# Kernel tuning notes

Measured on AMD Instinct MI355X. Metric: run time of the kernel, lower is better.

## Reference

```python
import jax, jax.numpy as jnp
import numpy as np

E = 500_000
N = 50_000
F_IN = 128
F_OUT = 128


def setup_inputs() -> dict:
    key = jax.random.key(0)
    ks = jax.random.split(key, 6)
    src_feat = jax.random.normal(ks[0], (E, F_IN), dtype=jnp.float32)
    dst_feat = jax.random.normal(ks[1], (E, F_IN), dtype=jnp.float32)
    # sorted dst ids -> contiguous per-dst segments (edges grouped by dst, time-ordered within group)
    dst_np = np.sort(np.random.default_rng(0).integers(0, N, size=E)).astype(np.int64)
    seg_start = np.searchsorted(dst_np, dst_np, side='left')  # first edge index of each edge's segment
    e_idx = np.arange(E)
    u = np.random.default_rng(1).random(E)
    # dst_max_eid: index of last edge (within same dst group) with time <= this edge's time
    dst_max_eid_np = (seg_start + np.floor(u * (e_idx - seg_start + 1))).astype(np.int64)
    dst_deg_np = (dst_max_eid_np - seg_start + 1).astype(np.float32)
    gain = float(np.sqrt(2.0))  # relu gain, xavier_uniform
    lim = gain * np.sqrt(6.0 / (F_IN + F_OUT))
    W_self = jax.random.uniform(ks[2], (F_IN, F_OUT), minval=-lim, maxval=lim, dtype=jnp.float32)
    W_neigh = jax.random.uniform(ks[3], (F_IN, F_OUT), minval=-lim, maxval=lim, dtype=jnp.float32)
    return {
        'src_feat': src_feat,
        'dst_feat': dst_feat,
        'dst_ids': jnp.asarray(dst_np),
        'dst_max_eid': jnp.asarray(dst_max_eid_np),
        'dst_deg': jnp.asarray(dst_deg_np),
        'W_self': W_self,
        'b_self': jnp.zeros((F_OUT,), jnp.float32),
        'W_neigh': W_neigh,
        'b_neigh': jnp.zeros((F_OUT,), jnp.float32),
    }


def _segmented_cumsum(x, seg_ids):
    # seg_ids sorted ascending; per-segment inclusive prefix sum over edge axis
    cs = jnp.cumsum(x, axis=0)                                   # [E, F]
    seg_start = jnp.searchsorted(seg_ids, seg_ids, side='left')  # [E]
    cs_pad = jnp.concatenate([jnp.zeros((1, x.shape[1]), x.dtype), cs], axis=0)
    return cs - cs_pad[seg_start]                                # subtract prefix before segment


def reference(src_feat, dst_feat, dst_ids, dst_max_eid, dst_deg, W_self, b_self, W_neigh, b_neigh):
    # group_apply_edges(group_by='dst'): cumsum of src_feat within each dst segment ('mean' aggr)
    h_feat = _segmented_cumsum(src_feat, dst_ids)          # [E, F_in]
    h_neigh = h_feat[dst_max_eid]                          # gather running aggregate per edge
    mean_cof = dst_deg + 1.0
    h_neigh = h_neigh / mean_cof[:, None]
    rst = (dst_feat @ W_self + b_self) + (h_neigh @ W_neigh + b_neigh)
    return rst
```

## Files before the change

### kernel.cpp

```cpp
#include <hip/hip_runtime.h>
#include <hip/hip_bf16.h>


#define FDIM 128
#define NNODES 50000

typedef __attribute__((ext_vector_type(4))) float f32x4;
typedef __attribute__((ext_vector_type(2))) float f32x2;
typedef __attribute__((ext_vector_type(8))) short bf16x8;

static __device__ __forceinline__ float bf2f(unsigned short u) {
  union { unsigned int i; float f; } v; v.i = ((unsigned int)u) << 16; return v.f;
}
static __device__ __forceinline__ unsigned short f2bf(float f) {
  union { float f; unsigned int i; } v; v.f = f;
  unsigned int x = v.i;
  return (unsigned short)((x + 0x7fffu + ((x >> 16) & 1u)) >> 16);
}

__global__ __launch_bounds__(256) void pack_w_kernel(
    const float* __restrict__ Wself,
    const float* __restrict__ Wneigh,
    unsigned short* __restrict__ Wp)
{
  int t = blockIdx.x * blockDim.x + threadIdx.x;
  if (t >= 8 * 8 * 64) return;
  int l  = t & 63;
  int n0 = (t >> 6) & 7;
  int ks = t >> 9;
  int n = n0 * 16 + (l & 15);
  int kbase = ks * 32 + ((l >> 4) * 8);
  unsigned short outv[8] __attribute__((aligned(16)));
#pragma unroll
  for (int j = 0; j < 8; ++j) {
    int k = kbase + j;
    float w = (k < FDIM) ? Wself[k * FDIM + n] : Wneigh[(k - FDIM) * FDIM + n];
    outv[j] = f2bf(w);
  }
  ((uint4*)Wp)[t] = *(const uint4*)outv;
}

__global__ __launch_bounds__(256) void seg_start_kernel(
    const int* __restrict__ dst_ids,
    int* __restrict__ node_start,
    int E, int nnodes)
{
  int e = blockIdx.x * blockDim.x + threadIdx.x;
  if (e >= E) return;
  int d = dst_ids[e];
  int dprev = (e == 0) ? -1 : dst_ids[e - 1];
  for (int n = dprev + 1; n <= d; ++n) node_start[n] = e;
  if (e == E - 1) {
    for (int n = d + 1; n <= nnodes; ++n) node_start[n] = E;
  }
}

__global__ __launch_bounds__(256) void seg_cumsum_kernel(
    const float* __restrict__ src,
    const int* __restrict__ node_start,
    unsigned short* __restrict__ cs,
    int nnodes)
{
  int wave = (blockIdx.x * blockDim.x + threadIdx.x) >> 6;
  int lane = threadIdx.x & 63;
  if (wave >= nnodes) return;

  int s = node_start[wave];
  int e = node_start[wave + 1];
  if (s >= e) return;

  const float* sp = src + (size_t)s * FDIM + lane * 2;
  unsigned int* op = (unsigned int*)(cs + (size_t)s * FDIM + lane * 2);

  f32x2 v0 = *(const f32x2*)sp;
  f32x2 v1 = (s + 1 < e) ? *(const f32x2*)(sp + FDIM) : v0;
  float a0 = 0.f, a1 = 0.f;
  for (int j = s; j < e; ++j) {
    f32x2 vn = v1;
    if (j + 2 < e) vn = *(const f32x2*)(sp + (size_t)(j + 2 - s) * FDIM);
    a0 += v0.x;
    a1 += v0.y;
    unsigned int w = ((unsigned int)f2bf(a1) << 16) | (unsigned int)f2bf(a0);
    *op = w;
    op += FDIM / 2;
    v0 = v1;
    v1 = vn;
  }
}

__global__ __launch_bounds__(256) void gemm_kernel(
    const float* __restrict__ dstf,
    const unsigned short* __restrict__ cs,
    const int* __restrict__ dst_max_eid,
    const float* __restrict__ dst_deg,
    const unsigned short* __restrict__ Wp,
    const float* __restrict__ b_self,
    const float* __restrict__ b_neigh,
    float* __restrict__ out,
    int E)
{
  int lane = threadIdx.x & 63;
  int wave = threadIdx.x >> 6;
  int quad = lane >> 4;
  int lnib = lane & 15;
  int m0 = blockIdx.x * 64 + wave * 16;
  int row = m0 + lnib;
  int rclamp = (row < E) ? row : (E - 1);

  bf16x8 afrag[8];
  const float* arow = dstf + (size_t)rclamp * FDIM + quad * 8;
#pragma unroll
  for (int ks = 0; ks < 4; ++ks) {
    f32x4 lo = *(const f32x4*)(arow + ks * 32);
    f32x4 hi = *(const f32x4*)(arow + ks * 32 + 4);
    bf16x8 a;
#pragma unroll
    for (int j = 0; j < 4; ++j) {
      a[j]     = (short)f2bf(lo[j]);
      a[4 + j] = (short)f2bf(hi[j]);
    }
    afrag[ks] = a;
  }

  int eid = dst_max_eid[rclamp];
  float invc = 1.0f / (dst_deg[rclamp] + 1.0f);
  const unsigned short* nrow = cs + (size_t)eid * FDIM + quad * 8;
#pragma unroll
  for (int ks = 0; ks < 4; ++ks) {
    bf16x8 raw = *(const bf16x8*)(nrow + ks * 32);
    bf16x8 sc;
#pragma unroll
    for (int j = 0; j < 8; ++j)
      sc[j] = (short)f2bf(bf2f((unsigned short)raw[j]) * invc);
    afrag[4 + ks] = sc;
  }

  f32x4 acc[8];
#pragma unroll
  for (int n0 = 0; n0 < 8; ++n0) acc[n0] = (f32x4){0.f, 0.f, 0.f, 0.f};

  const bf16x8* wpv = (const bf16x8*)Wp;
#pragma unroll
  for (int ks = 0; ks < 8; ++ks) {
#pragma unroll
    for (int n0 = 0; n0 < 8; ++n0) {
      bf16x8 b = wpv[(ks * 8 + n0) * 64 + lane];
      acc[n0] = __builtin_amdgcn_mfma_f32_16x16x32_bf16(afrag[ks], b, acc[n0], 0, 0, 0);
    }
  }

#pragma unroll
  for (int n0 = 0; n0 < 8; ++n0) {
    int n = n0 * 16 + lnib;
    float bias = b_self[n] + b_neigh[n];
#pragma unroll
    for (int r = 0; r < 4; ++r) {
      int orow = m0 + quad * 4 + r;
      if (orow < E)
        out[(size_t)orow * FDIM + n] = acc[n0][r] + bias;
    }
  }
}

extern "C" void kernel_launch(void* const* d_in, const int* in_sizes, int n_in,
                              void* d_out, int out_size, void* d_ws, size_t ws_size,
                              hipStream_t stream) {
  const float* src_feat    = (const float*)d_in[0];
  const float* dst_feat    = (const float*)d_in[1];
  const int*   dst_ids     = (const int*)d_in[2];
  const int*   dst_max_eid = (const int*)d_in[3];
  const float* dst_deg     = (const float*)d_in[4];
  const float* W_self      = (const float*)d_in[5];
  const float* b_self      = (const float*)d_in[6];
  const float* W_neigh     = (const float*)d_in[7];
  const float* b_neigh     = (const float*)d_in[8];

  int E = in_sizes[0] / FDIM;

  unsigned short* Wp = (unsigned short*)d_ws;
  unsigned short* cs = (unsigned short*)((char*)d_ws + 65536);

  int* node_start = (int*)d_out;

  pack_w_kernel<<<16, 256, 0, stream>>>(W_self, W_neigh, Wp);

  int sblocks = (E + 255) / 256;
  seg_start_kernel<<<sblocks, 256, 0, stream>>>(dst_ids, node_start, E, NNODES);

  int nwaves_blocks = (NNODES * 64 + 255) / 256;
  seg_cumsum_kernel<<<nwaves_blocks, 256, 0, stream>>>(src_feat, node_start, cs, NNODES);

  int gblocks = (E + 63) / 64;
  gemm_kernel<<<gblocks, 256, 0, stream>>>(dst_feat, cs, dst_max_eid, dst_deg, Wp,
                                           b_self, b_neigh, (float*)d_out, E);
}
```

Before: 686.8 us.

## Deepen cumsum prefetch and double GEMM rows per wave with B-fragment reuse

The segmented cumsum kernel now keeps four rows in flight instead of two, so more loads are outstanding while the serial accumulation runs. The GEMM kernel gives each wave 32 rows (two 16-row MFMA tiles), so every weight fragment loaded is used twice. It also loops over output column blocks with the next block's weights prefetched, issues the neighbour gathers early, and skips the bounds checks on full tiles. This cuts weight load traffic and hides gather latency, at the cost of more registers and therefore possibly lower occupancy.

```diff
diff --git a/kernel.cpp b/kernel.cpp
--- a/kernel.cpp
+++ b/kernel.cpp
@@ -67,25 +67,35 @@
 
   int s = node_start[wave];
   int e = node_start[wave + 1];
-  if (s >= e) return;
+  int n = e - s;
+  if (n <= 0) return;
 
   const float* sp = src + (size_t)s * FDIM + lane * 2;
   unsigned int* op = (unsigned int*)(cs + (size_t)s * FDIM + lane * 2);
 
+  f32x2 z = {0.f, 0.f};
   f32x2 v0 = *(const f32x2*)sp;
-  f32x2 v1 = (s + 1 < e) ? *(const f32x2*)(sp + FDIM) : v0;
+  f32x2 v1 = (n > 1) ? *(const f32x2*)(sp + FDIM) : z;
+  f32x2 v2 = (n > 2) ? *(const f32x2*)(sp + 2 * FDIM) : z;
+  f32x2 v3 = (n > 3) ? *(const f32x2*)(sp + 3 * FDIM) : z;
+
   float a0 = 0.f, a1 = 0.f;
-  for (int j = s; j < e; ++j) {
-    f32x2 vn = v1;
-    if (j + 2 < e) vn = *(const f32x2*)(sp + (size_t)(j + 2 - s) * FDIM);
-    a0 += v0.x;
-    a1 += v0.y;
-    unsigned int w = ((unsigned int)f2bf(a1) << 16) | (unsigned int)f2bf(a0);
-    *op = w;
-    op += FDIM / 2;
-    v0 = v1;
-    v1 = vn;
-  }
+  int k = 0;
+#define CS_STEP(V)                                                              \
+  {                                                                             \
+    a0 += V.x; a1 += V.y;                                                       \
+    *op = ((unsigned int)f2bf(a1) << 16) | (unsigned int)f2bf(a0);              \
+    op += FDIM / 2;                                                             \
+    if (++k == n) break;                                                        \
+    if (k + 3 < n) V = *(const f32x2*)(sp + (size_t)(k + 3) * FDIM);            \
+  }
+  while (true) {
+    CS_STEP(v0)
+    CS_STEP(v1)
+    CS_STEP(v2)
+    CS_STEP(v3)
+  }
+#undef CS_STEP
 }
 
 __global__ __launch_bounds__(256) void gemm_kernel(
@@ -103,61 +113,127 @@
   int wave = threadIdx.x >> 6;
   int quad = lane >> 4;
   int lnib = lane & 15;
-  int m0 = blockIdx.x * 64 + wave * 16;
-  int row = m0 + lnib;
-  int rclamp = (row < E) ? row : (E - 1);
-
-  bf16x8 afrag[8];
-  const float* arow = dstf + (size_t)rclamp * FDIM + quad * 8;
-#pragma unroll
-  for (int ks = 0; ks < 4; ++ks) {
-    f32x4 lo = *(const f32x4*)(arow + ks * 32);
-    f32x4 hi = *(const f32x4*)(arow + ks * 32 + 4);
+  int m0 = blockIdx.x * 128 + wave * 32;
+
+  int r0 = m0 + lnib;
+  int r1 = m0 + 16 + lnib;
+  int rc0 = (r0 < E) ? r0 : E - 1;
+  int rc1 = (r1 < E) ? r1 : E - 1;
+
+  int eid0 = dst_max_eid[rc0];
+  int eid1 = dst_max_eid[rc1];
+  float invc0 = 1.0f / (dst_deg[rc0] + 1.0f);
+  float invc1 = 1.0f / (dst_deg[rc1] + 1.0f);
+
+  const unsigned short* nrow0 = cs + (size_t)eid0 * FDIM + quad * 8;
+  const unsigned short* nrow1 = cs + (size_t)eid1 * FDIM + quad * 8;
+  bf16x8 raw0_0 = *(const bf16x8*)(nrow0);
+  bf16x8 raw0_1 = *(const bf16x8*)(nrow0 + 32);
+  bf16x8 raw0_2 = *(const bf16x8*)(nrow0 + 64);
+  bf16x8 raw0_3 = *(const bf16x8*)(nrow0 + 96);
+  bf16x8 raw1_0 = *(const bf16x8*)(nrow1);
+  bf16x8 raw1_1 = *(const bf16x8*)(nrow1 + 32);
+  bf16x8 raw1_2 = *(const bf16x8*)(nrow1 + 64);
+  bf16x8 raw1_3 = *(const bf16x8*)(nrow1 + 96);
+
+  const float* arow0 = dstf + (size_t)rc0 * FDIM + quad * 8;
+  const float* arow1 = dstf + (size_t)rc1 * FDIM + quad * 8;
+
+  bf16x8 afrag0[8], afrag1[8];
+#pragma unroll
+  for (int ks = 0; ks < 4; ++ks) {
+    f32x4 lo = *(const f32x4*)(arow0 + ks * 32);
+    f32x4 hi = *(const f32x4*)(arow0 + ks * 32 + 4);
     bf16x8 a;
 #pragma unroll
     for (int j = 0; j < 4; ++j) {
       a[j]     = (short)f2bf(lo[j]);
       a[4 + j] = (short)f2bf(hi[j]);
     }
-    afrag[ks] = a;
-  }
-
-  int eid = dst_max_eid[rclamp];
-  float invc = 1.0f / (dst_deg[rclamp] + 1.0f);
-  const unsigned short* nrow = cs + (size_t)eid * FDIM + quad * 8;
-#pragma unroll
-  for (int ks = 0; ks < 4; ++ks) {
-    bf16x8 raw = *(const bf16x8*)(nrow + ks * 32);
+    afrag0[ks] = a;
+  }
+#pragma unroll
+  for (int ks = 0; ks < 4; ++ks) {
+    f32x4 lo = *(const f32x4*)(arow1 + ks * 32);
+    f32x4 hi = *(const f32x4*)(arow1 + ks * 32 + 4);
+    bf16x8 a;
+#pragma unroll
+    for (int j = 0; j < 4; ++j) {
+      a[j]     = (short)f2bf(lo[j]);
+      a[4 + j] = (short)f2bf(hi[j]);
+    }
+    afrag1[ks] = a;
+  }
+
+  float bias_r[8];
+#pragma unroll
+  for (int n0 = 0; n0 < 8; ++n0)
+    bias_r[n0] = b_self[n0 * 16 + lnib] + b_neigh[n0 * 16 + lnib];
+
+#pragma unroll
+  for (int ks = 0; ks < 4; ++ks) {
+    bf16x8 raw = (ks == 0) ? raw0_0 : (ks == 1) ? raw0_1 : (ks == 2) ? raw0_2 : raw0_3;
     bf16x8 sc;
 #pragma unroll
     for (int j = 0; j < 8; ++j)
-      sc[j] = (short)f2bf(bf2f((unsigned short)raw[j]) * invc);
-    afrag[4 + ks] = sc;
-  }
-
-  f32x4 acc[8];
-#pragma unroll
-  for (int n0 = 0; n0 < 8; ++n0) acc[n0] = (f32x4){0.f, 0.f, 0.f, 0.f};
+      sc[j] = (short)f2bf(bf2f((unsigned short)raw[j]) * invc0);
+    afrag0[4 + ks] = sc;
+  }
+#pragma unroll
+  for (int ks = 0; ks < 4; ++ks) {
+    bf16x8 raw = (ks == 0) ? raw1_0 : (ks == 1) ? raw1_1 : (ks == 2) ? raw1_2 : raw1_3;
+    bf16x8 sc;
+#pragma unroll
+    for (int j = 0; j < 8; ++j)
+      sc[j] = (short)f2bf(bf2f((unsigned short)raw[j]) * invc1);
+    afrag1[4 + ks] = sc;
+  }
 
   const bf16x8* wpv = (const bf16x8*)Wp;
-#pragma unroll
-  for (int ks = 0; ks < 8; ++ks) {
-#pragma unroll
-    for (int n0 = 0; n0 < 8; ++n0) {
-      bf16x8 b = wpv[(ks * 8 + n0) * 64 + lane];
-      acc[n0] = __builtin_amdgcn_mfma_f32_16x16x32_bf16(afrag[ks], b, acc[n0], 0, 0, 0);
-    }
-  }
+  bool full = (m0 + 32 <= E);
+
+  bf16x8 bcur[8];
+#pragma unroll
+  for (int ks = 0; ks < 8; ++ks) bcur[ks] = wpv[ks * 512 + lane];
 
 #pragma unroll
   for (int n0 = 0; n0 < 8; ++n0) {
+    bf16x8 bnext[8];
+    if (n0 < 7) {
+#pragma unroll
+      for (int ks = 0; ks < 8; ++ks)
+        bnext[ks] = wpv[(ks * 8 + n0 + 1) * 64 + lane];
+    }
+
+    f32x4 a0 = (f32x4){0.f, 0.f, 0.f, 0.f};
+    f32x4 a1 = (f32x4){0.f, 0.f, 0.f, 0.f};
+#pragma unroll
+    for (int ks = 0; ks < 8; ++ks) {
+      a0 = __builtin_amdgcn_mfma_f32_16x16x32_bf16(afrag0[ks], bcur[ks], a0, 0, 0, 0);
+      a1 = __builtin_amdgcn_mfma_f32_16x16x32_bf16(afrag1[ks], bcur[ks], a1, 0, 0, 0);
+    }
+
     int n = n0 * 16 + lnib;
-    float bias = b_self[n] + b_neigh[n];
-#pragma unroll
-    for (int r = 0; r < 4; ++r) {
-      int orow = m0 + quad * 4 + r;
-      if (orow < E)
-        out[(size_t)orow * FDIM + n] = acc[n0][r] + bias;
+    float bias = bias_r[n0];
+    if (full) {
+#pragma unroll
+      for (int r = 0; r < 4; ++r) {
+        out[(size_t)(m0 + quad * 4 + r) * FDIM + n]      = a0[r] + bias;
+        out[(size_t)(m0 + 16 + quad * 4 + r) * FDIM + n] = a1[r] + bias;
+      }
+    } else {
+#pragma unroll
+      for (int r = 0; r < 4; ++r) {
+        int o0 = m0 + quad * 4 + r;
+        int o1 = m0 + 16 + quad * 4 + r;
+        if (o0 < E) out[(size_t)o0 * FDIM + n] = a0[r] + bias;
+        if (o1 < E) out[(size_t)o1 * FDIM + n] = a1[r] + bias;
+      }
+    }
+
+    if (n0 < 7) {
+#pragma unroll
+      for (int ks = 0; ks < 8; ++ks) bcur[ks] = bnext[ks];
     }
   }
 }
@@ -190,7 +266,7 @@
   int nwaves_blocks = (NNODES * 64 + 255) / 256;
   seg_cumsum_kernel<<<nwaves_blocks, 256, 0, stream>>>(src_feat, node_start, cs, NNODES);
 
-  int gblocks = (E + 63) / 64;
+  int gblocks = (E + 127) / 128;
   gemm_kernel<<<gblocks, 256, 0, stream>>>(dst_feat, cs, dst_max_eid, dst_deg, Wp,
                                            b_self, b_neigh, (float*)d_out, E);
 }
```

New measurement: 644.9 us. 6.1% less time.
